# Kernel optimization log

Hardware: AMD Instinct MI355X
Metric: run time of the kernel (lower is better)

## Reference

```python
import jax, jax.numpy as jnp
import numpy as np

EPS = 1e-5
GROUPS = 32


def setup_inputs() -> dict:
    key = jax.random.key(0)
    ks = jax.random.split(key, 12)
    b, c, h, w = 8, 256, 64, 64
    s = 1.0 / np.sqrt(c)
    return {
        "x": jax.random.normal(ks[0], (b, c, h, w), jnp.float32),
        "gn_w": jax.random.uniform(ks[1], (c,), jnp.float32, 0.5, 1.5),
        "gn_b": jax.random.normal(ks[2], (c,), jnp.float32) * 0.1,
        "wq": jax.random.normal(ks[3], (c, c), jnp.float32) * s,
        "bq": jax.random.normal(ks[4], (c,), jnp.float32) * 0.02,
        "wk": jax.random.normal(ks[5], (c, c), jnp.float32) * s,
        "bk": jax.random.normal(ks[6], (c,), jnp.float32) * 0.02,
        "wv": jax.random.normal(ks[7], (c, c), jnp.float32) * s,
        "bv": jax.random.normal(ks[8], (c,), jnp.float32) * 0.02,
        "wp": jax.random.normal(ks[9], (c, c), jnp.float32) * s,
        "bp": jax.random.normal(ks[10], (c,), jnp.float32) * 0.02,
        "gamma": jax.random.normal(ks[11], (1,), jnp.float32),
    }


def _group_norm(x, weight, bias):
    b, c, h, w = x.shape
    g = min(c, GROUPS)
    xg = x.reshape(b, g, c // g, h * w)
    mean = xg.mean(axis=(2, 3), keepdims=True)
    var = jnp.var(xg, axis=(2, 3), keepdims=True)
    xn = (xg - mean) * jax.lax.rsqrt(var + EPS)
    xn = xn.reshape(b, c, h, w)
    return xn * weight[None, :, None, None] + bias[None, :, None, None]


def reference(x, gn_w, gn_b, wq, bq, wk, bk, wv, bv, wp, bp, gamma):
    b, c, h, w = x.shape
    x_dash = _group_norm(x, gn_w, gn_b)           # (b,c,h,w)
    xf = x_dash.reshape(b, c, h * w)              # (b,c,n)
    # 1x1 convs == per-pixel linear maps over channels
    q = jnp.einsum('oc,bcn->bon', wq, xf) + bq[None, :, None]
    k = jnp.einsum('oc,bcn->bon', wk, xf) + bk[None, :, None]
    v = jnp.einsum('oc,bcn->bon', wv, xf) + bv[None, :, None]
    # attn[b,i,j] = <q[:,i], k[:,j]> / sqrt(c)
    attn = jnp.einsum('bci,bcj->bij', q, k) / jnp.sqrt(jnp.asarray(c, x.dtype))
    attn = jax.nn.softmax(attn, axis=-1)
    # out[b,c,i] = sum_j v[b,c,j] * attn[b,i,j]
    out = jnp.einsum('bcj,bij->bci', v, attn)
    out = jnp.einsum('oc,bcn->bon', wp, out) + bp[None, :, None]
    out = out.reshape(b, c, h, w)
    return x + gamma[0] * out
```

## Files before the change

kernel.cpp:

```cpp
#include <hip/hip_runtime.h>
#include <cstdint>
#include <cstddef>


#define NB   8
#define NC   256
#define NPIX 4096
#define CPG  8

typedef __attribute__((ext_vector_type(8))) short bf16x8;
typedef __attribute__((ext_vector_type(4))) short s16x4;
typedef __attribute__((ext_vector_type(8))) short s16x8;
typedef __attribute__((ext_vector_type(4))) float f32x4;

__device__ __forceinline__ short f2bf(float f) {
  union { float f; uint32_t u; } v; v.f = f;
  return (short)((v.u + 0x7fffu + ((v.u >> 16) & 1u)) >> 16);
}

__device__ __forceinline__ uint32_t cvtpk_bf(float a, float b) {
  uint32_t r;
  asm("v_cvt_pk_bf16_f32 %0, %1, %2" : "=v"(r) : "v"(a), "v"(b));
  return r;
}

__device__ __forceinline__ f32x4 mfma16(bf16x8 a, bf16x8 b, f32x4 c) {
  return __builtin_amdgcn_mfma_f32_16x16x32_bf16(a, b, c, 0, 0, 0);
}

__device__ __forceinline__ void gload_lds16(const short* g, short* l) {
  __builtin_amdgcn_global_load_lds(
      (const __attribute__((address_space(1))) void*)g,
      (__attribute__((address_space(3))) void*)l, 16, 0, 0);
}

__global__ __launch_bounds__(256) void wconv4(
    const float* __restrict__ w0, const float* __restrict__ w1,
    const float* __restrict__ w2, const float* __restrict__ w3,
    short* __restrict__ o0, short* __restrict__ o1,
    short* __restrict__ o2, short* __restrict__ o3) {
  int m = blockIdx.x >> 6;
  const float* w = (m == 0) ? w0 : (m == 1) ? w1 : (m == 2) ? w2 : w3;
  short* o = (m == 0) ? o0 : (m == 1) ? o1 : (m == 2) ? o2 : o3;
  int i = ((blockIdx.x & 63) * 256 + threadIdx.x) * 4;
  float4 v = *reinterpret_cast<const float4*>(w + i);
  s16x4 p;
  p[0] = f2bf(v.x); p[1] = f2bf(v.y); p[2] = f2bf(v.z); p[3] = f2bf(v.w);
  *reinterpret_cast<s16x4*>(o + i) = p;
}

__global__ __launch_bounds__(1024) void gnorm(const float* __restrict__ x,
                                              const float* __restrict__ gw,
                                              const float* __restrict__ gb,
                                              short* __restrict__ xdt) {
  int b = blockIdx.x >> 5;
  int g = blockIdx.x & 31;
  const float* xp = x + ((size_t)b * NC + (size_t)g * CPG) * NPIX;
  int t = threadIdx.x;

  float s = 0.f, ss = 0.f;
  const float4* xp4 = reinterpret_cast<const float4*>(xp);
  for (int i = t; i < (CPG * NPIX) / 4; i += 1024) {
    float4 v = xp4[i];
    s  += v.x + v.y + v.z + v.w;
    ss += v.x * v.x + v.y * v.y + v.z * v.z + v.w * v.w;
  }
  for (int m = 32; m; m >>= 1) { s += __shfl_xor(s, m); ss += __shfl_xor(ss, m); }
  __shared__ float red[34];
  int wid = t >> 6;
  if ((t & 63) == 0) { red[wid] = s; red[16 + wid] = ss; }
  __syncthreads();
  if (t == 0) {
    float a = 0.f, b2 = 0.f;
    for (int i = 0; i < 16; ++i) { a += red[i]; b2 += red[16 + i]; }
    float mean = a * (1.f / 32768.f);
    float var  = b2 * (1.f / 32768.f) - mean * mean;
    red[32] = mean;
    red[33] = rsqrtf(var + 1e-5f);
  }
  __syncthreads();
  float mean = red[32], rstd = red[33];

  float wv2[CPG], bv2[CPG];
  for (int cc = 0; cc < CPG; ++cc) {
    float wgt = gw[g * CPG + cc] * rstd;
    wv2[cc] = wgt;
    bv2[cc] = gb[g * CPG + cc] - mean * wgt;
  }
  for (int pix = t; pix < NPIX; pix += 1024) {
    s16x8 pk;
    for (int cc = 0; cc < CPG; ++cc)
      pk[cc] = f2bf(fmaf(xp[cc * NPIX + pix], wv2[cc], bv2[cc]));
    *reinterpret_cast<s16x8*>(&xdt[((size_t)b * NPIX + pix) * NC + g * CPG]) = pk;
  }
}

__global__ __launch_bounds__(256) void qkv_gemm(
    const short* __restrict__ wq_bf, const short* __restrict__ wk_bf,
    const short* __restrict__ wv_bf,
    const float* __restrict__ bq, const float* __restrict__ bk,
    const float* __restrict__ bv,
    const short* __restrict__ xdt,
    short* __restrict__ qt, short* __restrict__ kt, short* __restrict__ vv) {
  int nt = blockIdx.x, b = blockIdx.y;

  __shared__ short xtile[64 * 256];
  __shared__ float bias_lds[3][256];
  int t = threadIdx.x;
  const short* xg = xdt + ((size_t)b * NPIX + nt * 64) * NC;
  for (int it = 0; it < 8; ++it) {
    int id = t + it * 256, row = id >> 5, part = id & 31;
    *reinterpret_cast<uint4*>(&xtile[row * 256 + (part ^ (row & 7)) * 8]) =
        *reinterpret_cast<const uint4*>(&xg[(size_t)row * 256 + part * 8]);
  }
  bias_lds[0][t] = bq[t];
  bias_lds[1][t] = bk[t];
  bias_lds[2][t] = bv[t];
  __syncthreads();

  int w = t >> 6, lane = t & 63, g = lane >> 4, lr = lane & 15;
  const short* Ws[3] = {wq_bf, wk_bf, wv_bf};

  for (int mi = 0; mi < 3; ++mi) {
    const short* W = Ws[mi];
    f32x4 acc[4][4];
    f32x4 zz = {0.f, 0.f, 0.f, 0.f};
    for (int i = 0; i < 4; ++i) for (int j = 0; j < 4; ++j) acc[i][j] = zz;

    for (int c0 = 0; c0 < 256; c0 += 32) {
      bf16x8 af[4], bfr[4];
      for (int mf = 0; mf < 4; ++mf)
        af[mf] = *reinterpret_cast<const bf16x8*>(
            &W[(size_t)(w * 64 + mf * 16 + lr) * 256 + c0 + g * 8]);
      for (int nf = 0; nf < 4; ++nf) {
        int row = nf * 16 + lr;
        bfr[nf] = *reinterpret_cast<const bf16x8*>(
            &xtile[row * 256 + (((c0 >> 3) + g) ^ (row & 7)) * 8]);
      }
      for (int mf = 0; mf < 4; ++mf)
        for (int nf = 0; nf < 4; ++nf)
          acc[mf][nf] = mfma16(af[mf], bfr[nf], acc[mf][nf]);
    }

    if (mi < 2) {
      short* outp = (mi == 0) ? qt : kt;
      for (int mf = 0; mf < 4; ++mf)
        for (int nf = 0; nf < 4; ++nf) {
          int ob = w * 64 + mf * 16 + g * 4;
          int n  = nt * 64 + nf * 16 + lr;
          s16x4 pk;
          for (int r = 0; r < 4; ++r)
            pk[r] = f2bf(acc[mf][nf][r] + bias_lds[mi][ob + r]);
          *reinterpret_cast<s16x4*>(&outp[((size_t)b * NPIX + n) * NC + ob]) = pk;
        }
    } else {
      for (int mf = 0; mf < 4; ++mf)
        for (int nf = 0; nf < 4; ++nf) {
          int ob = w * 64 + mf * 16 + g * 4;
          int n  = nt * 64 + nf * 16 + lr;
          for (int r = 0; r < 4; ++r)
            vv[((size_t)b * NC + ob + r) * NPIX + n] =
                f2bf(acc[mf][nf][r] + bias_lds[2][ob + r]);
        }
    }
  }
}

__global__ __launch_bounds__(256, 2) void attn(
    const short* __restrict__ qt, const short* __restrict__ kt,
    const short* __restrict__ vv, short* __restrict__ ot) {
  int b = blockIdx.x, itile = blockIdx.y;
  __shared__ short ktile[64 * 256];
  __shared__ short Pb[2][64 * 64];
  __shared__ float lfin[2][64];

  int t = threadIdx.x, w = t >> 6, lane = t & 63, g = lane >> 4, lr = lane & 15;
  int kk = w >> 1, qq = w & 1;
  int i0 = itile * 64;

  const short* ktg = kt + (size_t)b * NPIX * NC;

  for (int it = 0; it < 8; ++it) {
    int id = it * 256 + t, row = id >> 5, ch = id & 31;
    gload_lds16(ktg + row * 256 + (ch ^ (row & 7)) * 8, &ktile[id * 8]);
  }
  const short* kgp = ktg + 16384;

  bf16x8 qf[2][8];
  for (int qi = 0; qi < 2; ++qi) {
    const short* qrow =
        qt + ((size_t)b * NPIX + i0 + 32 * qq + 16 * qi + lr) * NC;
    for (int ks = 0; ks < 8; ++ks)
      qf[qi][ks] = *reinterpret_cast<const bf16x8*>(&qrow[ks * 32 + g * 8]);
  }

  const short* vbase =
      vv + (size_t)b * NC * NPIX + (size_t)(w * 64 + lr) * NPIX + g * 8;

  int row0 = 32 * kk + lr, row1 = row0 + 16;
  int pwo[2][2];
  for (int qi = 0; qi < 2; ++qi) {
    int q_loc = 32 * qq + 16 * qi + lr;
    for (int mt = 0; mt < 2; ++mt)
      pwo[qi][mt] = q_loc * 64 +
                    (((4 * kk + 2 * mt + (g >> 1)) ^ (q_loc & 7)) * 8) +
                    (g & 1) * 4;
  }
  int pr[4][2];
  for (int nf = 0; nf < 4; ++nf)
    for (int ks2 = 0; ks2 < 2; ++ks2) {
      int qc = nf * 16 + lr;
      pr[nf][ks2] = qc * 64 + (((ks2 * 4 + g) ^ (qc & 7)) * 8);
    }

  f32x4 zz = {0.f, 0.f, 0.f, 0.f};
  f32x4 oacc[4][4];
  for (int i = 0; i < 4; ++i) for (int j = 0; j < 4; ++j) oacc[i][j] = zz;
  bf16x8 va0[4], va1[4];
  float l_p[2] = {0.f, 0.f};

  const float sc = 0.0625f, L2E = 1.44269504f;
  const float SCL = sc * L2E;

  for (int jt = 0; jt < 64; ++jt) {
    int cur = jt & 1, prv = cur ^ 1;

    asm volatile("s_waitcnt vmcnt(0) lgkmcnt(0)" ::: "memory");
    __builtin_amdgcn_s_barrier();
    asm volatile("" ::: "memory");

    if (jt > 0) {
      __builtin_amdgcn_s_setprio(1);
      bf16x8 pb[4];
#pragma unroll
      for (int nf = 0; nf < 4; ++nf)
        pb[nf] = *reinterpret_cast<const bf16x8*>(&Pb[prv][pr[nf][0]]);
#pragma unroll
      for (int mf = 0; mf < 4; ++mf)
#pragma unroll
        for (int nf = 0; nf < 4; ++nf)
          oacc[mf][nf] = mfma16(va0[mf], pb[nf], oacc[mf][nf]);
      __builtin_amdgcn_s_setprio(0);
      const short* vp = vbase + (size_t)(jt - 1) * 64 + 32;
#pragma unroll
      for (int mf = 0; mf < 4; ++mf)
        va1[mf] = *reinterpret_cast<const bf16x8*>(vp + (size_t)mf * (16 * NPIX));
    }

    f32x4 s[2][2];
    s[0][0] = zz; s[0][1] = zz; s[1][0] = zz; s[1][1] = zz;
    __builtin_amdgcn_s_setprio(1);
#pragma unroll
    for (int ks = 0; ks < 8; ++ks) {
      bf16x8 kf0 = *reinterpret_cast<const bf16x8*>(
          &ktile[row0 * 256 + (((ks * 4) + g) ^ (row0 & 7)) * 8]);
      bf16x8 kf1 = *reinterpret_cast<const bf16x8*>(
          &ktile[row1 * 256 + (((ks * 4) + g) ^ (row1 & 7)) * 8]);
      s[0][0] = mfma16(kf0, qf[0][ks], s[0][0]);
      s[0][1] = mfma16(kf0, qf[1][ks], s[0][1]);
      s[1][0] = mfma16(kf1, qf[0][ks], s[1][0]);
      s[1][1] = mfma16(kf1, qf[1][ks], s[1][1]);
    }
    __builtin_amdgcn_s_setprio(0);

    asm volatile("s_waitcnt lgkmcnt(0)" ::: "memory");
    __builtin_amdgcn_s_barrier();
    asm volatile("" ::: "memory");

    for (int it = 0; it < 8; ++it) {
      int id = it * 256 + t, row = id >> 5, ch = id & 31;
      gload_lds16(kgp + row * 256 + (ch ^ (row & 7)) * 8, &ktile[id * 8]);
    }
    kgp += 16384;

    {
      const short* vp = vbase + (size_t)jt * 64;
#pragma unroll
      for (int mf = 0; mf < 4; ++mf)
        va0[mf] = *reinterpret_cast<const bf16x8*>(vp + (size_t)mf * (16 * NPIX));
    }

    if (jt > 0) {
      asm volatile("s_waitcnt vmcnt(12)" ::: "memory");
      __builtin_amdgcn_s_setprio(1);
      bf16x8 pb[4];
#pragma unroll
      for (int nf = 0; nf < 4; ++nf)
        pb[nf] = *reinterpret_cast<const bf16x8*>(&Pb[prv][pr[nf][1]]);
#pragma unroll
      for (int mf = 0; mf < 4; ++mf)
#pragma unroll
        for (int nf = 0; nf < 4; ++nf)
          oacc[mf][nf] = mfma16(va1[mf], pb[nf], oacc[mf][nf]);
      __builtin_amdgcn_s_setprio(0);
    }

#pragma unroll
    for (int qi = 0; qi < 2; ++qi) {
      float ps = 0.f;
#pragma unroll
      for (int mt = 0; mt < 2; ++mt) {
        float p0 = exp2f(s[mt][qi][0] * SCL);
        float p1 = exp2f(s[mt][qi][1] * SCL);
        float p2 = exp2f(s[mt][qi][2] * SCL);
        float p3 = exp2f(s[mt][qi][3] * SCL);
        ps += (p0 + p1) + (p2 + p3);
        uint2 pk;
        pk.x = cvtpk_bf(p0, p1);
        pk.y = cvtpk_bf(p2, p3);
        *reinterpret_cast<uint2*>(&Pb[cur][pwo[qi][mt]]) = pk;
      }
      l_p[qi] += ps;
    }
  }

  {
    const short* vp = vbase + (size_t)63 * 64 + 32;
#pragma unroll
    for (int mf = 0; mf < 4; ++mf)
      va1[mf] = *reinterpret_cast<const bf16x8*>(vp + (size_t)mf * (16 * NPIX));
  }
  asm volatile("s_waitcnt vmcnt(0) lgkmcnt(0)" ::: "memory");
  __builtin_amdgcn_s_barrier();
  asm volatile("" ::: "memory");
  {
    bf16x8 pb[4];
#pragma unroll
    for (int nf = 0; nf < 4; ++nf)
      pb[nf] = *reinterpret_cast<const bf16x8*>(&Pb[1][pr[nf][0]]);
    for (int mf = 0; mf < 4; ++mf)
      for (int nf = 0; nf < 4; ++nf)
        oacc[mf][nf] = mfma16(va0[mf], pb[nf], oacc[mf][nf]);
#pragma unroll
    for (int nf = 0; nf < 4; ++nf)
      pb[nf] = *reinterpret_cast<const bf16x8*>(&Pb[1][pr[nf][1]]);
    for (int mf = 0; mf < 4; ++mf)
      for (int nf = 0; nf < 4; ++nf)
        oacc[mf][nf] = mfma16(va1[mf], pb[nf], oacc[mf][nf]);
  }

#pragma unroll
  for (int qi = 0; qi < 2; ++qi) {
    float v = l_p[qi];
    v += __shfl_xor(v, 16);
    v += __shfl_xor(v, 32);
    l_p[qi] = v;
  }
  if (lane < 16) {
    lfin[kk][32 * qq + lr]      = l_p[0];
    lfin[kk][32 * qq + 16 + lr] = l_p[1];
  }
  __syncthreads();

  for (int nf = 0; nf < 4; ++nf) {
    int q = nf * 16 + lr;
    float inv = 1.f / (lfin[0][q] + lfin[1][q]);
    int i = i0 + q;
    for (int mf = 0; mf < 4; ++mf) {
      int cb = w * 64 + mf * 16 + g * 4;
      s16x4 pk;
      for (int r = 0; r < 4; ++r) pk[r] = f2bf(oacc[mf][nf][r] * inv);
      *reinterpret_cast<s16x4*>(&ot[((size_t)b * NPIX + i) * NC + cb]) = pk;
    }
  }
}

__global__ __launch_bounds__(256) void proj_res(
    const short* __restrict__ wp_bf, const float* __restrict__ bp,
    const short* __restrict__ ot, const float* __restrict__ x,
    const float* __restrict__ gamma, float* __restrict__ out) {
  int nt = blockIdx.x, b = blockIdx.y;
  __shared__ short otile[64 * 256];
  __shared__ float bias_lds[256];
  int t = threadIdx.x;
  const short* og = ot + ((size_t)b * NPIX + nt * 64) * NC;
  for (int itx = 0; itx < 8; ++itx) {
    int id = t + itx * 256, row = id >> 5, part = id & 31;
    *reinterpret_cast<uint4*>(&otile[row * 256 + (part ^ (row & 7)) * 8]) =
        *reinterpret_cast<const uint4*>(&og[(size_t)row * 256 + part * 8]);
  }
  bias_lds[t] = bp[t];
  __syncthreads();

  int w = t >> 6, lane = t & 63, g = lane >> 4, lr = lane & 15;
  f32x4 acc[4][4];
  f32x4 zz = {0.f, 0.f, 0.f, 0.f};
  for (int i = 0; i < 4; ++i) for (int j = 0; j < 4; ++j) acc[i][j] = zz;

  for (int c0 = 0; c0 < 256; c0 += 32) {
    bf16x8 af[4], bfr[4];
    for (int mf = 0; mf < 4; ++mf)
      af[mf] = *reinterpret_cast<const bf16x8*>(
          &wp_bf[(size_t)(w * 64 + mf * 16 + lr) * 256 + c0 + g * 8]);
    for (int nf = 0; nf < 4; ++nf) {
      int row = nf * 16 + lr;
      bfr[nf] = *reinterpret_cast<const bf16x8*>(
          &otile[row * 256 + (((c0 >> 3) + g) ^ (row & 7)) * 8]);
    }
    for (int mf = 0; mf < 4; ++mf)
      for (int nf = 0; nf < 4; ++nf)
        acc[mf][nf] = mfma16(af[mf], bfr[nf], acc[mf][nf]);
  }

  float gm = gamma[0];
  for (int mf = 0; mf < 4; ++mf)
    for (int nf = 0; nf < 4; ++nf) {
      int ob = w * 64 + mf * 16 + g * 4;
      int n  = nt * 64 + nf * 16 + lr;
      for (int r = 0; r < 4; ++r) {
        size_t idx = ((size_t)b * NC + ob + r) * NPIX + n;
        out[idx] = x[idx] + gm * (acc[mf][nf][r] + bias_lds[ob + r]);
      }
    }
}

extern "C" void kernel_launch(void* const* d_in, const int* in_sizes, int n_in,
                              void* d_out, int out_size, void* d_ws, size_t ws_size,
                              hipStream_t stream) {
  (void)in_sizes; (void)n_in; (void)out_size; (void)ws_size;
  const float* x     = (const float*)d_in[0];
  const float* gn_w  = (const float*)d_in[1];
  const float* gn_b  = (const float*)d_in[2];
  const float* wq    = (const float*)d_in[3];
  const float* bq    = (const float*)d_in[4];
  const float* wk    = (const float*)d_in[5];
  const float* bk    = (const float*)d_in[6];
  const float* wv    = (const float*)d_in[7];
  const float* bv    = (const float*)d_in[8];
  const float* wp    = (const float*)d_in[9];
  const float* bp    = (const float*)d_in[10];
  const float* gamma = (const float*)d_in[11];
  float* out = (float*)d_out;

  char* ws = (char*)d_ws;
  const size_t WSZ = 131072;
  const size_t TSZ = (size_t)NB * NPIX * NC * 2;
  short* wq_bf = (short*)(ws);
  short* wk_bf = (short*)(ws + WSZ);
  short* wv_bf = (short*)(ws + 2 * WSZ);
  short* wp_bf = (short*)(ws + 3 * WSZ);
  short* xdt   = (short*)(ws + 4 * WSZ);
  short* qt    = (short*)(ws + 4 * WSZ + TSZ);
  short* kt    = (short*)(ws + 4 * WSZ + 2 * TSZ);
  short* vv    = (short*)(ws + 4 * WSZ + 3 * TSZ);
  short* ot    = xdt;

  wconv4<<<256, 256, 0, stream>>>(wq, wk, wv, wp, wq_bf, wk_bf, wv_bf, wp_bf);

  gnorm<<<256, 1024, 0, stream>>>(x, gn_w, gn_b, xdt);

  qkv_gemm<<<dim3(64, 8), 256, 0, stream>>>(wq_bf, wk_bf, wv_bf, bq, bk, bv,
                                            xdt, qt, kt, vv);

  attn<<<dim3(8, 64), 256, 0, stream>>>(qt, kt, vv, ot);

  proj_res<<<dim3(64, 8), 256, 0, stream>>>(wp_bf, bp, ot, x, gamma, out);
}
```

Measured before the change: 270.5 us.

## Split attention key range across two blocks and merge partial outputs

Splits the key dimension of the attention kernel in two (grid z=2), so each block handles 32 key tiles and writes unnormalized bf16 partial outputs plus row sums. A new merge kernel adds the two partials and normalizes. This doubles the grid from 512 to 1024 blocks for better CU occupancy on the GPU. The cost is an extra kernel launch, extra global traffic for the partials, and bf16 rounding of the unnormalized partials. The P buffer is also reduced to a single LDS buffer with an added barrier, which cuts LDS use but adds synchronisation. The no-max softmax stays valid because exps are summed without a shift.

```diff
diff --git a/kernel.cpp b/kernel.cpp
--- a/kernel.cpp
+++ b/kernel.cpp
@@ -16,6 +16,12 @@
 __device__ __forceinline__ short f2bf(float f) {
   union { float f; uint32_t u; } v; v.f = f;
   return (short)((v.u + 0x7fffu + ((v.u >> 16) & 1u)) >> 16);
+}
+
+__device__ __forceinline__ float bf2f(short s) {
+  union { uint32_t u; float f; } v;
+  v.u = ((uint32_t)(unsigned short)s) << 16;
+  return v.f;
 }
 
 __device__ __forceinline__ uint32_t cvtpk_bf(float a, float b) {
@@ -168,10 +174,12 @@
 
 __global__ __launch_bounds__(256, 2) void attn(
     const short* __restrict__ qt, const short* __restrict__ kt,
-    const short* __restrict__ vv, short* __restrict__ ot) {
-  int b = blockIdx.x, itile = blockIdx.y;
+    const short* __restrict__ vv, short* __restrict__ outp,
+    float* __restrict__ lp, int njt, int final_write) {
+  int b = blockIdx.x, itile = blockIdx.y, kh = blockIdx.z;
+  int jt0 = kh * njt;
   __shared__ short ktile[64 * 256];
-  __shared__ short Pb[2][64 * 64];
+  __shared__ short Pb[64 * 64];
   __shared__ float lfin[2][64];
 
   int t = threadIdx.x, w = t >> 6, lane = t & 63, g = lane >> 4, lr = lane & 15;
@@ -180,11 +188,20 @@
 
   const short* ktg = kt + (size_t)b * NPIX * NC;
 
+  int dmaSrc[8], dmaDst[8];
+#pragma unroll
   for (int it = 0; it < 8; ++it) {
     int id = it * 256 + t, row = id >> 5, ch = id & 31;
-    gload_lds16(ktg + row * 256 + (ch ^ (row & 7)) * 8, &ktile[id * 8]);
-  }
-  const short* kgp = ktg + 16384;
+    dmaSrc[it] = row * 256 + (ch ^ (row & 7)) * 8;
+    dmaDst[it] = id * 8;
+  }
+
+  {
+    const short* kb = ktg + (size_t)jt0 * 16384;
+#pragma unroll
+    for (int it = 0; it < 8; ++it) gload_lds16(kb + dmaSrc[it], &ktile[dmaDst[it]]);
+  }
+  const short* kgp = ktg + (size_t)(jt0 + 1) * 16384;
 
   bf16x8 qf[2][8];
   for (int qi = 0; qi < 2; ++qi) {
@@ -222,19 +239,19 @@
   const float sc = 0.0625f, L2E = 1.44269504f;
   const float SCL = sc * L2E;
 
-  for (int jt = 0; jt < 64; ++jt) {
-    int cur = jt & 1, prv = cur ^ 1;
+  for (int j = 0; j < njt; ++j) {
+    int jt = jt0 + j;
 
     asm volatile("s_waitcnt vmcnt(0) lgkmcnt(0)" ::: "memory");
     __builtin_amdgcn_s_barrier();
     asm volatile("" ::: "memory");
 
-    if (jt > 0) {
+    if (j > 0) {
       __builtin_amdgcn_s_setprio(1);
       bf16x8 pb[4];
 #pragma unroll
       for (int nf = 0; nf < 4; ++nf)
-        pb[nf] = *reinterpret_cast<const bf16x8*>(&Pb[prv][pr[nf][0]]);
+        pb[nf] = *reinterpret_cast<const bf16x8*>(&Pb[pr[nf][0]]);
 #pragma unroll
       for (int mf = 0; mf < 4; ++mf)
 #pragma unroll
@@ -267,10 +284,9 @@
     __builtin_amdgcn_s_barrier();
     asm volatile("" ::: "memory");
 
-    for (int it = 0; it < 8; ++it) {
-      int id = it * 256 + t, row = id >> 5, ch = id & 31;
-      gload_lds16(kgp + row * 256 + (ch ^ (row & 7)) * 8, &ktile[id * 8]);
-    }
+#pragma unroll
+    for (int it = 0; it < 8; ++it)
+      gload_lds16(kgp + dmaSrc[it], &ktile[dmaDst[it]]);
     kgp += 16384;
 
     {
@@ -280,13 +296,13 @@
         va0[mf] = *reinterpret_cast<const bf16x8*>(vp + (size_t)mf * (16 * NPIX));
     }
 
-    if (jt > 0) {
+    if (j > 0) {
       asm volatile("s_waitcnt vmcnt(12)" ::: "memory");
       __builtin_amdgcn_s_setprio(1);
       bf16x8 pb[4];
 #pragma unroll
       for (int nf = 0; nf < 4; ++nf)
-        pb[nf] = *reinterpret_cast<const bf16x8*>(&Pb[prv][pr[nf][1]]);
+        pb[nf] = *reinterpret_cast<const bf16x8*>(&Pb[pr[nf][1]]);
 #pragma unroll
       for (int mf = 0; mf < 4; ++mf)
 #pragma unroll
@@ -294,6 +310,10 @@
           oacc[mf][nf] = mfma16(va1[mf], pb[nf], oacc[mf][nf]);
       __builtin_amdgcn_s_setprio(0);
     }
+
+    asm volatile("s_waitcnt lgkmcnt(0)" ::: "memory");
+    __builtin_amdgcn_s_barrier();
+    asm volatile("" ::: "memory");
 
 #pragma unroll
     for (int qi = 0; qi < 2; ++qi) {
@@ -308,14 +328,14 @@
         uint2 pk;
         pk.x = cvtpk_bf(p0, p1);
         pk.y = cvtpk_bf(p2, p3);
-        *reinterpret_cast<uint2*>(&Pb[cur][pwo[qi][mt]]) = pk;
+        *reinterpret_cast<uint2*>(&Pb[pwo[qi][mt]]) = pk;
       }
       l_p[qi] += ps;
     }
   }
 
   {
-    const short* vp = vbase + (size_t)63 * 64 + 32;
+    const short* vp = vbase + (size_t)(jt0 + njt - 1) * 64 + 32;
 #pragma unroll
     for (int mf = 0; mf < 4; ++mf)
       va1[mf] = *reinterpret_cast<const bf16x8*>(vp + (size_t)mf * (16 * NPIX));
@@ -327,13 +347,13 @@
     bf16x8 pb[4];
 #pragma unroll
     for (int nf = 0; nf < 4; ++nf)
-      pb[nf] = *reinterpret_cast<const bf16x8*>(&Pb[1][pr[nf][0]]);
+      pb[nf] = *reinterpret_cast<const bf16x8*>(&Pb[pr[nf][0]]);
     for (int mf = 0; mf < 4; ++mf)
       for (int nf = 0; nf < 4; ++nf)
         oacc[mf][nf] = mfma16(va0[mf], pb[nf], oacc[mf][nf]);
 #pragma unroll
     for (int nf = 0; nf < 4; ++nf)
-      pb[nf] = *reinterpret_cast<const bf16x8*>(&Pb[1][pr[nf][1]]);
+      pb[nf] = *reinterpret_cast<const bf16x8*>(&Pb[pr[nf][1]]);
     for (int mf = 0; mf < 4; ++mf)
       for (int nf = 0; nf < 4; ++nf)
         oacc[mf][nf] = mfma16(va1[mf], pb[nf], oacc[mf][nf]);
@@ -352,17 +372,41 @@
   }
   __syncthreads();
 
+  short* okh = outp + (size_t)kh * NB * NPIX * NC;
   for (int nf = 0; nf < 4; ++nf) {
     int q = nf * 16 + lr;
-    float inv = 1.f / (lfin[0][q] + lfin[1][q]);
+    float inv = final_write ? 1.f / (lfin[0][q] + lfin[1][q]) : 1.f;
     int i = i0 + q;
     for (int mf = 0; mf < 4; ++mf) {
       int cb = w * 64 + mf * 16 + g * 4;
       s16x4 pk;
       for (int r = 0; r < 4; ++r) pk[r] = f2bf(oacc[mf][nf][r] * inv);
-      *reinterpret_cast<s16x4*>(&ot[((size_t)b * NPIX + i) * NC + cb]) = pk;
-    }
-  }
+      *reinterpret_cast<s16x4*>(&okh[((size_t)b * NPIX + i) * NC + cb]) = pk;
+    }
+  }
+  if (!final_write && w < 2 && lane < 16) {
+    float* lk = lp + (size_t)kh * NB * NPIX + (size_t)b * NPIX + i0;
+#pragma unroll
+    for (int qi = 0; qi < 2; ++qi) {
+      int q = 32 * w + 16 * qi + lane;
+      lk[q] = lfin[0][q] + lfin[1][q];
+    }
+  }
+}
+
+__global__ __launch_bounds__(256) void attn_merge(
+    const short* __restrict__ o0, const short* __restrict__ o1,
+    const float* __restrict__ lp, short* __restrict__ ot) {
+  int idx = (blockIdx.x * 256 + threadIdx.x) * 8;
+  int row = idx >> 8;
+  float inv = 1.f / (lp[row] + lp[NB * NPIX + row]);
+  s16x8 a = *reinterpret_cast<const s16x8*>(o0 + idx);
+  s16x8 c = *reinterpret_cast<const s16x8*>(o1 + idx);
+  s16x8 o;
+#pragma unroll
+  for (int e = 0; e < 8; ++e)
+    o[e] = f2bf((bf2f(a[e]) + bf2f(c[e])) * inv);
+  *reinterpret_cast<s16x8*>(ot + idx) = o;
 }
 
 __global__ __launch_bounds__(256) void proj_res(
@@ -417,7 +461,7 @@
 extern "C" void kernel_launch(void* const* d_in, const int* in_sizes, int n_in,
                               void* d_out, int out_size, void* d_ws, size_t ws_size,
                               hipStream_t stream) {
-  (void)in_sizes; (void)n_in; (void)out_size; (void)ws_size;
+  (void)in_sizes; (void)n_in; (void)out_size;
   const float* x     = (const float*)d_in[0];
   const float* gn_w  = (const float*)d_in[1];
   const float* gn_b  = (const float*)d_in[2];
@@ -444,6 +488,9 @@
   short* kt    = (short*)(ws + 4 * WSZ + 2 * TSZ);
   short* vv    = (short*)(ws + 4 * WSZ + 3 * TSZ);
   short* ot    = xdt;
+  short* opart = (short*)(ws + 4 * WSZ + 4 * TSZ);
+  float* lpb   = (float*)(ws + 4 * WSZ + 6 * TSZ);
+  const size_t NEED = 4 * WSZ + 6 * TSZ + (size_t)2 * NB * NPIX * sizeof(float);
 
   wconv4<<<256, 256, 0, stream>>>(wq, wk, wv, wp, wq_bf, wk_bf, wv_bf, wp_bf);
 
@@ -452,7 +499,13 @@
   qkv_gemm<<<dim3(64, 8), 256, 0, stream>>>(wq_bf, wk_bf, wv_bf, bq, bk, bv,
                                             xdt, qt, kt, vv);
 
-  attn<<<dim3(8, 64), 256, 0, stream>>>(qt, kt, vv, ot);
+  if (ws_size >= NEED) {
+    attn<<<dim3(8, 64, 2), 256, 0, stream>>>(qt, kt, vv, opart, lpb, 32, 0);
+    attn_merge<<<4096, 256, 0, stream>>>(opart, opart + (size_t)NB * NPIX * NC,
+                                         lpb, ot);
+  } else {
+    attn<<<dim3(8, 64, 1), 256, 0, stream>>>(qt, kt, vv, ot, lpb, 64, 1);
+  }
 
   proj_res<<<dim3(64, 8), 256, 0, stream>>>(wp_bf, bp, ot, x, gamma, out);
 }
```

Measured after the change: 289.8 us. 1.07x slower.

## Share K tile across two query tiles per 512-thread attention block

Applied to the files above, without the earlier changes.

The attention kernel now launches 512-thread blocks, and each one processes two 64-row query tiles. The two groups of four waves share a single LDS K tile, so each block issues half as many K loads per thread, and total K traffic from global memory to LDS is halved. Pb and lfin are duplicated per sub-tile, and the vmcnt wait threshold is adjusted to match the smaller number of outstanding loads. The trade-off is that eight waves now synchronise at every barrier, and with higher LDS use per block fewer blocks may fit on each CU.

```diff
diff --git a/kernel.cpp b/kernel.cpp
--- a/kernel.cpp
+++ b/kernel.cpp
@@ -166,22 +166,24 @@
   }
 }
 
-__global__ __launch_bounds__(256, 2) void attn(
+__global__ __launch_bounds__(512, 2) void attn(
     const short* __restrict__ qt, const short* __restrict__ kt,
     const short* __restrict__ vv, short* __restrict__ ot) {
-  int b = blockIdx.x, itile = blockIdx.y;
+  int b = blockIdx.x;
   __shared__ short ktile[64 * 256];
-  __shared__ short Pb[2][64 * 64];
-  __shared__ float lfin[2][64];
+  __shared__ short Pb[2][2][64 * 64];
+  __shared__ float lfin[2][2][64];
 
   int t = threadIdx.x, w = t >> 6, lane = t & 63, g = lane >> 4, lr = lane & 15;
-  int kk = w >> 1, qq = w & 1;
+  int sub = w >> 2, wl = w & 3;
+  int kk = wl >> 1, qq = wl & 1;
+  int itile = blockIdx.y * 2 + sub;
   int i0 = itile * 64;
 
   const short* ktg = kt + (size_t)b * NPIX * NC;
 
-  for (int it = 0; it < 8; ++it) {
-    int id = it * 256 + t, row = id >> 5, ch = id & 31;
+  for (int it = 0; it < 4; ++it) {
+    int id = it * 512 + t, row = id >> 5, ch = id & 31;
     gload_lds16(ktg + row * 256 + (ch ^ (row & 7)) * 8, &ktile[id * 8]);
   }
   const short* kgp = ktg + 16384;
@@ -195,7 +197,7 @@
   }
 
   const short* vbase =
-      vv + (size_t)b * NC * NPIX + (size_t)(w * 64 + lr) * NPIX + g * 8;
+      vv + (size_t)b * NC * NPIX + (size_t)(wl * 64 + lr) * NPIX + g * 8;
 
   int row0 = 32 * kk + lr, row1 = row0 + 16;
   int pwo[2][2];
@@ -234,7 +236,7 @@
       bf16x8 pb[4];
 #pragma unroll
       for (int nf = 0; nf < 4; ++nf)
-        pb[nf] = *reinterpret_cast<const bf16x8*>(&Pb[prv][pr[nf][0]]);
+        pb[nf] = *reinterpret_cast<const bf16x8*>(&Pb[sub][prv][pr[nf][0]]);
 #pragma unroll
       for (int mf = 0; mf < 4; ++mf)
 #pragma unroll
@@ -267,8 +269,9 @@
     __builtin_amdgcn_s_barrier();
     asm volatile("" ::: "memory");
 
-    for (int it = 0; it < 8; ++it) {
-      int id = it * 256 + t, row = id >> 5, ch = id & 31;
+#pragma unroll
+    for (int it = 0; it < 4; ++it) {
+      int id = it * 512 + t, row = id >> 5, ch = id & 31;
       gload_lds16(kgp + row * 256 + (ch ^ (row & 7)) * 8, &ktile[id * 8]);
     }
     kgp += 16384;
@@ -281,12 +284,12 @@
     }
 
     if (jt > 0) {
-      asm volatile("s_waitcnt vmcnt(12)" ::: "memory");
+      asm volatile("s_waitcnt vmcnt(8)" ::: "memory");
       __builtin_amdgcn_s_setprio(1);
       bf16x8 pb[4];
 #pragma unroll
       for (int nf = 0; nf < 4; ++nf)
-        pb[nf] = *reinterpret_cast<const bf16x8*>(&Pb[prv][pr[nf][1]]);
+        pb[nf] = *reinterpret_cast<const bf16x8*>(&Pb[sub][prv][pr[nf][1]]);
 #pragma unroll
       for (int mf = 0; mf < 4; ++mf)
 #pragma unroll
@@ -308,7 +311,7 @@
         uint2 pk;
         pk.x = cvtpk_bf(p0, p1);
         pk.y = cvtpk_bf(p2, p3);
-        *reinterpret_cast<uint2*>(&Pb[cur][pwo[qi][mt]]) = pk;
+        *reinterpret_cast<uint2*>(&Pb[sub][cur][pwo[qi][mt]]) = pk;
       }
       l_p[qi] += ps;
     }
@@ -327,13 +330,13 @@
     bf16x8 pb[4];
 #pragma unroll
     for (int nf = 0; nf < 4; ++nf)
-      pb[nf] = *reinterpret_cast<const bf16x8*>(&Pb[1][pr[nf][0]]);
+      pb[nf] = *reinterpret_cast<const bf16x8*>(&Pb[sub][1][pr[nf][0]]);
     for (int mf = 0; mf < 4; ++mf)
       for (int nf = 0; nf < 4; ++nf)
         oacc[mf][nf] = mfma16(va0[mf], pb[nf], oacc[mf][nf]);
 #pragma unroll
     for (int nf = 0; nf < 4; ++nf)
-      pb[nf] = *reinterpret_cast<const bf16x8*>(&Pb[1][pr[nf][1]]);
+      pb[nf] = *reinterpret_cast<const bf16x8*>(&Pb[sub][1][pr[nf][1]]);
     for (int mf = 0; mf < 4; ++mf)
       for (int nf = 0; nf < 4; ++nf)
         oacc[mf][nf] = mfma16(va1[mf], pb[nf], oacc[mf][nf]);
@@ -347,17 +350,17 @@
     l_p[qi] = v;
   }
   if (lane < 16) {
-    lfin[kk][32 * qq + lr]      = l_p[0];
-    lfin[kk][32 * qq + 16 + lr] = l_p[1];
+    lfin[sub][kk][32 * qq + lr]      = l_p[0];
+    lfin[sub][kk][32 * qq + 16 + lr] = l_p[1];
   }
   __syncthreads();
 
   for (int nf = 0; nf < 4; ++nf) {
     int q = nf * 16 + lr;
-    float inv = 1.f / (lfin[0][q] + lfin[1][q]);
+    float inv = 1.f / (lfin[sub][0][q] + lfin[sub][1][q]);
     int i = i0 + q;
     for (int mf = 0; mf < 4; ++mf) {
-      int cb = w * 64 + mf * 16 + g * 4;
+      int cb = wl * 64 + mf * 16 + g * 4;
       s16x4 pk;
       for (int r = 0; r < 4; ++r) pk[r] = f2bf(oacc[mf][nf][r] * inv);
       *reinterpret_cast<s16x4*>(&ot[((size_t)b * NPIX + i) * NC + cb]) = pk;
@@ -452,7 +455,7 @@
   qkv_gemm<<<dim3(64, 8), 256, 0, stream>>>(wq_bf, wk_bf, wv_bf, bq, bk, bv,
                                             xdt, qt, kt, vv);
 
-  attn<<<dim3(8, 64), 256, 0, stream>>>(qt, kt, vv, ot);
+  attn<<<dim3(8, 32), 512, 0, stream>>>(qt, kt, vv, ot);
 
   proj_res<<<dim3(64, 8), 256, 0, stream>>>(wp_bf, bp, ot, x, gamma, out);
 }
```

Result: slower. 291.6 us (+7.8%).
